# Kernel tuning notes

Hardware: AMD Instinct MI355X
Metric: run time of the kernel (lower is better)

## Reference

```python
import jax, jax.numpy as jnp
import numpy as np

N = 50000        # nodes
E = 800000       # edges
F_IN = 128       # input_nf == output_nf
HID = 128        # hidden_nf
HEADS = 4
HD = HID // HEADS            # 32 per-head hidden
FEAT = 2 * F_IN + 1 + 1 + 1 + 9   # 268 edge feature dim


def setup_inputs() -> dict:
    key = jax.random.key(0)
    ks = jax.random.split(key, 16)
    f32 = jnp.float32
    inp = {}
    inp["h"] = jax.random.normal(ks[0], (N, F_IN), dtype=f32)
    inp["coord"] = jax.random.normal(ks[1], (N, 3), dtype=f32)
    inp["edge_index"] = jax.random.randint(ks[2], (2, E), 0, N, dtype=jnp.int64 if jax.config.read('jax_enable_x64') else jnp.int32)
    # per-head edge MLP: Linear(FEAT,HD) -> SiLU -> Linear(HD,HD), stacked over heads
    inp["eW1"] = jax.random.normal(ks[3], (HEADS, FEAT, HD), dtype=f32) / np.sqrt(FEAT)
    inp["eb1"] = jnp.zeros((HEADS, HD), dtype=f32)
    inp["eW2"] = jax.random.normal(ks[4], (HEADS, HD, HD), dtype=f32) / np.sqrt(HD)
    inp["eb2"] = jnp.zeros((HEADS, HD), dtype=f32)
    # LayerNorm over hidden_nf
    inp["ln_g"] = jnp.ones((HID,), dtype=f32)
    inp["ln_b"] = jnp.zeros((HID,), dtype=f32)
    # node_mlp: Linear(HID+F_IN, HID) -> SiLU -> Linear(HID, F_IN)
    inp["nW1"] = jax.random.normal(ks[5], (HID + F_IN, HID), dtype=f32) / np.sqrt(HID + F_IN)
    inp["nb1"] = jnp.zeros((HID,), dtype=f32)
    inp["nW2"] = jax.random.normal(ks[6], (HID, F_IN), dtype=f32) / np.sqrt(HID)
    inp["nb2"] = jnp.zeros((F_IN,), dtype=f32)
    # coord_mlp: Linear(HID, HID) -> SiLU -> Linear(HID, 1, bias=False, xavier gain=0.001)
    inp["cW1"] = jax.random.normal(ks[7], (HID, HID), dtype=f32) / np.sqrt(HID)
    inp["cb1"] = jnp.zeros((HID,), dtype=f32)
    inp["cW2"] = jax.random.normal(ks[8], (HID, 1), dtype=f32) * 0.001
    return inp


def _forward(h, coord, edge_index, eW1, eb1, eW2, eb2, ln_g, ln_b,
             nW1, nb1, nW2, nb2, cW1, cb1, cW2):
    eps, thr = 1e-8, 1e-6
    row, col = edge_index[0], edge_index[1]
    n = h.shape[0]
    ci = coord[row]            # [E,3]
    ck = coord[col]            # [E,3]
    coord_diff = ci - ck       # rel_coord, also used for coord update
    radial = jnp.sum(coord_diff * coord_diff, axis=-1, keepdims=True)   # [E,1]
    dist = jnp.sqrt(radial)                                             # ||rel_coord||
    dot = jnp.sum(ci * ck, axis=-1, keepdims=True)                      # [E,1]
    # SO3 frame per edge
    a = coord_diff / (jnp.linalg.norm(coord_diff, axis=1, keepdims=True) + eps)
    cp = jnp.cross(ci, ck)
    b = cp / (jnp.linalg.norm(cp, axis=1, keepdims=True) + eps)
    c = jnp.cross(a, b)
    mask = ((jnp.linalg.norm(a, axis=1) < thr) |
            (jnp.linalg.norm(b, axis=1) < thr) |
            (jnp.linalg.norm(c, axis=1) < thr))
    so3 = jnp.stack([a, b, c], axis=2)                                  # [E,3,3] columns a,b,c
    so3 = jnp.where(mask[:, None, None], jnp.eye(3, dtype=so3.dtype), so3)
    so3_flat = so3.reshape(-1, 9)
    # edge features -> per-head small MLPs
    feats = jnp.concatenate([h[row], h[col], radial, dist, dot, so3_flat], axis=1)  # [E,FEAT]
    x = jax.nn.silu(jnp.einsum('ef,hfd->hed', feats, eW1) + eb1[:, None, :])
    x = jnp.einsum('hed,hdk->hek', x, eW2) + eb2[:, None, :]            # [H,E,HD]
    edge_feat = jnp.transpose(x, (1, 0, 2)).reshape(x.shape[1], -1)     # [E,HID], head-major concat
    # LayerNorm
    mu = edge_feat.mean(axis=-1, keepdims=True)
    var = edge_feat.var(axis=-1, keepdims=True)
    edge_feat = (edge_feat - mu) / jnp.sqrt(var + 1e-5) * ln_g + ln_b
    # coord update
    w = jax.nn.silu(edge_feat @ cW1 + cb1) @ cW2                        # [E,1]
    trans = coord_diff * w
    coord_out = coord + jax.ops.segment_sum(trans, row, num_segments=n)
    # node update
    agg = jax.ops.segment_sum(edge_feat, row, num_segments=n)           # [N,HID]
    y = jax.nn.silu(jnp.concatenate([h, agg], axis=1) @ nW1 + nb1) @ nW2 + nb2
    h_out = h + y                                                       # residual
    return h_out, coord_out


def reference(h, coord, edge_index, eW1, eb1, eW2, eb2, ln_g, ln_b,
              nW1, nb1, nW2, nb2, cW1, cb1, cW2):
    return _forward(h, coord, edge_index, eW1, eb1, eW2, eb2, ln_g, ln_b,
                    nW1, nb1, nW2, nb2, cW1, cb1, cW2)
```

## Files before the change

### kernel.cpp

```cpp
#include <hip/hip_runtime.h>
#include <hip/hip_bf16.h>
#include <math.h>

#define NN 50000
#define EE 800000
#define FIN 128
#define HIDN 128
#define HD 32
#define FEATD 268
#define K1 288
#define KP1 296
#define TE 64
#define TN2 64

typedef __bf16 bf16x8 __attribute__((ext_vector_type(8)));
typedef __bf16 bf16x4 __attribute__((ext_vector_type(4)));
typedef float  f32x4  __attribute__((ext_vector_type(4)));

#define MFMA(a, b, c) __builtin_amdgcn_mfma_f32_16x16x32_bf16((a), (b), (c), 0, 0, 0)

__device__ __forceinline__ float silu_f(float x) {
    return x / (1.0f + __expf(-x));
}

__global__ void wconv_kernel(const float* __restrict__ eW1, const float* __restrict__ eW2,
                             const float* __restrict__ cW1, const float* __restrict__ nW1,
                             const float* __restrict__ nW2,
                             __bf16* __restrict__ eW1t, __bf16* __restrict__ eW2t,
                             __bf16* __restrict__ cW1t, __bf16* __restrict__ nW1t,
                             __bf16* __restrict__ nW2t)
{
    const int i = blockIdx.x * 256 + threadIdx.x;
    if (i < 4 * 32 * K1) {
        const int hh = i / (32 * K1), rs = i % (32 * K1), d = rs / K1, k = rs % K1;
        const float v = (k < FEATD) ? eW1[(size_t)hh * FEATD * HD + (size_t)k * HD + d] : 0.f;
        eW1t[i] = (__bf16)v;
    }
    if (i < 4 * HD * HD) {
        const int hh = i / (HD * HD), rs = i % (HD * HD), d = rs / HD, k = rs % HD;
        eW2t[i] = (__bf16)eW2[(size_t)hh * HD * HD + (size_t)k * HD + d];
    }
    if (i < HIDN * HIDN) {
        const int o = i / HIDN, k = i % HIDN;
        cW1t[i] = (__bf16)cW1[(size_t)k * HIDN + o];
    }
    if (i < HIDN * (2 * FIN)) {
        const int o = i / (2 * FIN), k = i % (2 * FIN);
        nW1t[i] = (__bf16)nW1[(size_t)k * HIDN + o];
    }
    if (i < FIN * HIDN) {
        const int o = i / HIDN, k = i % HIDN;
        nW2t[i] = (__bf16)nW2[(size_t)k * FIN + o];
    }
}

__global__ __launch_bounds__(256) void hconv_kernel(const float* __restrict__ h,
                                                    float* __restrict__ houtbase)
{
    const int i = blockIdx.x * 256 + threadIdx.x;
    if (i >= NN * FIN / 8) return;
    const int row = i >> 4;
    const int c8  = i & 15;
    const float4* src = (const float4*)(h + (size_t)row * FIN + c8 * 8);
    float4 a = src[0], b = src[1];
    bf16x8 v = { (__bf16)a.x, (__bf16)a.y, (__bf16)a.z, (__bf16)a.w,
                 (__bf16)b.x, (__bf16)b.y, (__bf16)b.z, (__bf16)b.w };
    *(bf16x8*)((char*)houtbase + (size_t)row * 512 + c8 * 16) = v;
}

__global__ __launch_bounds__(512) void edge_kernel(
    const float* __restrict__ coord,
    const int* __restrict__ ei,
    const __bf16* __restrict__ eW1t, const float* __restrict__ eb1,
    const __bf16* __restrict__ eW2t, const float* __restrict__ eb2,
    const float* __restrict__ ln_g, const float* __restrict__ ln_b,
    const __bf16* __restrict__ cW1t, const float* __restrict__ cb1,
    const float* __restrict__ cW2,
    float* __restrict__ houtbase, float* __restrict__ coord_out)
{
    __shared__ __align__(16) unsigned char smemA[TE * KP1 * 2];
    __shared__ __align__(16) unsigned char smemB[4 * TE * 40 * 2];
    __shared__ float cdiff[TE][3];
    __shared__ int   rowlds[TE];
    __shared__ float wsum[TE];

    __bf16 (*featsB)[KP1] = (__bf16 (*)[KP1])smemA;
    float  (*efs)[132]    = (float  (*)[132])smemA;
    __bf16 (*efsB)[136]   = (__bf16 (*)[136])smemB;

    const int t  = threadIdx.x;
    const int e0 = blockIdx.x * TE;

    if (t < TE) wsum[t] = 0.f;

    {
        const int e = t >> 3;
        const int q = t & 7;
        const int r = ei[e0 + e];
        const int c = ei[EE + e0 + e];
        #pragma unroll
        for (int j = 0; j < 2; j++) {
            const int c16 = q + 8 * j;
            uint4 vr = *(const uint4*)((const char*)houtbase + (size_t)r * 512 + c16 * 16);
            *(uint4*)&featsB[e][c16 * 8] = vr;
            uint4 vc = *(const uint4*)((const char*)houtbase + (size_t)c * 512 + c16 * 16);
            *(uint4*)&featsB[e][FIN + c16 * 8] = vc;
        }
        if (q == 0) {
            rowlds[e] = r;
            const float cix = coord[(size_t)r*3+0], ciy = coord[(size_t)r*3+1], ciz = coord[(size_t)r*3+2];
            const float ckx = coord[(size_t)c*3+0], cky = coord[(size_t)c*3+1], ckz = coord[(size_t)c*3+2];
            const float dx = cix-ckx, dy = ciy-cky, dz = ciz-ckz;
            cdiff[e][0]=dx; cdiff[e][1]=dy; cdiff[e][2]=dz;
            const float radial = dx*dx + dy*dy + dz*dz;
            const float dist   = sqrtf(radial);
            const float dotv   = cix*ckx + ciy*cky + ciz*ckz;
            const float ia = 1.0f / (dist + 1e-8f);
            float ax = dx*ia, ay = dy*ia, az = dz*ia;
            const float cpx = ciy*ckz - ciz*cky;
            const float cpy = ciz*ckx - cix*ckz;
            const float cpz = cix*cky - ciy*ckx;
            const float cpn = sqrtf(cpx*cpx + cpy*cpy + cpz*cpz);
            const float ib = 1.0f / (cpn + 1e-8f);
            float bx = cpx*ib, by = cpy*ib, bz = cpz*ib;
            float cx = ay*bz - az*by;
            float cy = az*bx - ax*bz;
            float cz = ax*by - ay*bx;
            const float na = sqrtf(ax*ax + ay*ay + az*az);
            const float nb = sqrtf(bx*bx + by*by + bz*bz);
            const float nc = sqrtf(cx*cx + cy*cy + cz*cz);
            if (na < 1e-6f || nb < 1e-6f || nc < 1e-6f) {
                ax=1.f; bx=0.f; cx=0.f;
                ay=0.f; by=1.f; cy=0.f;
                az=0.f; bz=0.f; cz=1.f;
            }
            featsB[e][256]=(__bf16)radial; featsB[e][257]=(__bf16)dist; featsB[e][258]=(__bf16)dotv;
            featsB[e][259]=(__bf16)ax; featsB[e][260]=(__bf16)bx; featsB[e][261]=(__bf16)cx;
            featsB[e][262]=(__bf16)ay; featsB[e][263]=(__bf16)by; featsB[e][264]=(__bf16)cy;
            featsB[e][265]=(__bf16)az; featsB[e][266]=(__bf16)bz; featsB[e][267]=(__bf16)cz;
            #pragma unroll
            for (int k = FEATD; k < K1; k++) featsB[e][k] = (__bf16)0.f;
        }
    }
    __syncthreads();

    const int wv2  = t >> 6;
    const int hh   = wv2 >> 1;
    const int mh   = wv2 & 1;
    const int lane = t & 63;
    const int lr   = lane & 15;
    const int lg   = lane >> 4;

    __bf16* hidB = ((__bf16*)smemB) + hh * (TE * 40);

    const f32x4 z4 = { 0.f, 0.f, 0.f, 0.f };

    {
        f32x4 acc[2][2];
        #pragma unroll
        for (int mti = 0; mti < 2; mti++) { acc[mti][0] = z4; acc[mti][1] = z4; }
        const __bf16* W1 = eW1t + (size_t)hh * 32 * K1;
        #pragma unroll
        for (int ks = 0; ks < 9; ks++) {
            const int kof = ks * 32 + lg * 8;
            bf16x8 b0 = *(const bf16x8*)(W1 + (size_t)lr * K1 + kof);
            bf16x8 b1 = *(const bf16x8*)(W1 + (size_t)(16 + lr) * K1 + kof);
            #pragma unroll
            for (int mti = 0; mti < 2; mti++) {
                bf16x8 a = *(const bf16x8*)(&featsB[(mh * 2 + mti) * 16 + lr][kof]);
                acc[mti][0] = MFMA(a, b0, acc[mti][0]);
                acc[mti][1] = MFMA(a, b1, acc[mti][1]);
            }
        }
        const float b1a = eb1[hh * HD + lr];
        const float b1b = eb1[hh * HD + 16 + lr];
        #pragma unroll
        for (int mti = 0; mti < 2; mti++) {
            #pragma unroll
            for (int r = 0; r < 4; r++) {
                const int erow = (mh * 2 + mti) * 16 + lg * 4 + r;
                hidB[erow * 40 + lr]      = (__bf16)silu_f(acc[mti][0][r] + b1a);
                hidB[erow * 40 + 16 + lr] = (__bf16)silu_f(acc[mti][1][r] + b1b);
            }
        }
    }
    __syncthreads();

    {
        f32x4 acc2[2][2];
        #pragma unroll
        for (int mti = 0; mti < 2; mti++) { acc2[mti][0] = z4; acc2[mti][1] = z4; }
        const __bf16* W2 = eW2t + (size_t)hh * HD * HD;
        const int kof2 = lg * 8;
        bf16x8 b20 = *(const bf16x8*)(W2 + (size_t)lr * HD + kof2);
        bf16x8 b21 = *(const bf16x8*)(W2 + (size_t)(16 + lr) * HD + kof2);
        #pragma unroll
        for (int mti = 0; mti < 2; mti++) {
            bf16x8 a = *(const bf16x8*)(hidB + ((mh * 2 + mti) * 16 + lr) * 40 + kof2);
            acc2[mti][0] = MFMA(a, b20, acc2[mti][0]);
            acc2[mti][1] = MFMA(a, b21, acc2[mti][1]);
        }
        const float b2a = eb2[hh * HD + lr];
        const float b2b = eb2[hh * HD + 16 + lr];
        #pragma unroll
        for (int mti = 0; mti < 2; mti++) {
            #pragma unroll
            for (int r = 0; r < 4; r++) {
                const int erow = (mh * 2 + mti) * 16 + lg * 4 + r;
                efs[erow][hh * HD + lr]      = acc2[mti][0][r] + b2a;
                efs[erow][hh * HD + 16 + lr] = acc2[mti][1][r] + b2b;
            }
        }
    }
    __syncthreads();

    {
        const int el = t >> 3;
        const int q8 = t & 7;
        float s = 0.f, s2 = 0.f;
        #pragma unroll
        for (int i = 0; i < 16; i++) {
            const float v = efs[el][q8 + 8 * i];
            s += v; s2 += v * v;
        }
        s  += __shfl_xor(s, 1);  s  += __shfl_xor(s, 2);  s  += __shfl_xor(s, 4);
        s2 += __shfl_xor(s2, 1); s2 += __shfl_xor(s2, 2); s2 += __shfl_xor(s2, 4);
        const float mu   = s * (1.f / 128.f);
        const float var  = s2 * (1.f / 128.f) - mu * mu;
        const float rstd = rsqrtf(var + 1e-5f);
        #pragma unroll
        for (int i = 0; i < 16; i++) {
            const int oo = q8 + 8 * i;
            const float v  = efs[el][oo];
            const float nv = (v - mu) * rstd * ln_g[oo] + ln_b[oo];
            efsB[el][oo] = (__bf16)nv;
        }
    }
    __syncthreads();

    {
        f32x4 acc3[2][2];
        #pragma unroll
        for (int mti = 0; mti < 2; mti++) { acc3[mti][0] = z4; acc3[mti][1] = z4; }
        const __bf16* W3 = cW1t + (size_t)hh * 32 * HIDN;
        #pragma unroll
        for (int ks = 0; ks < 4; ks++) {
            const int kof = ks * 32 + lg * 8;
            bf16x8 b30 = *(const bf16x8*)(W3 + (size_t)lr * HIDN + kof);
            bf16x8 b31 = *(const bf16x8*)(W3 + (size_t)(16 + lr) * HIDN + kof);
            #pragma unroll
            for (int mti = 0; mti < 2; mti++) {
                bf16x8 a = *(const bf16x8*)(&efsB[(mh * 2 + mti) * 16 + lr][kof]);
                acc3[mti][0] = MFMA(a, b30, acc3[mti][0]);
                acc3[mti][1] = MFMA(a, b31, acc3[mti][1]);
            }
        }
        const int c0 = hh * 32 + lr, c1 = c0 + 16;
        const float cbA = cb1[c0], cbB = cb1[c1];
        const float cwA = cW2[c0], cwB = cW2[c1];
        float pe[8];
        #pragma unroll
        for (int mti = 0; mti < 2; mti++)
            #pragma unroll
            for (int r = 0; r < 4; r++)
                pe[mti * 4 + r] = silu_f(acc3[mti][0][r] + cbA) * cwA
                                + silu_f(acc3[mti][1][r] + cbB) * cwB;
        #pragma unroll
        for (int d = 1; d < 16; d <<= 1)
            #pragma unroll
            for (int i = 0; i < 8; i++) pe[i] += __shfl_xor(pe[i], d);
        if (lr == 0) {
            #pragma unroll
            for (int mti = 0; mti < 2; mti++)
                #pragma unroll
                for (int r = 0; r < 4; r++)
                    atomicAdd(&wsum[(mh * 2 + mti) * 16 + lg * 4 + r], pe[mti * 4 + r]);
        }
    }
    __syncthreads();

    if (t < TE) {
        const float we = wsum[t];
        const int r = rowlds[t];
        atomicAdd(&coord_out[(size_t)r*3+0], cdiff[t][0] * we);
        atomicAdd(&coord_out[(size_t)r*3+1], cdiff[t][1] * we);
        atomicAdd(&coord_out[(size_t)r*3+2], cdiff[t][2] * we);
    }

    {
        const int p  = t & 63;
        const int gq = t >> 6;
        #pragma unroll
        for (int e2 = 0; e2 < 8; e2++) {
            const int ee = gq * 8 + e2;
            __hip_bfloat162 pk = *(__hip_bfloat162*)&efsB[ee][2 * p];
            __hip_bfloat162* addr = (__hip_bfloat162*)
                ((char*)houtbase + (size_t)rowlds[ee] * 512 + 256 + p * 4);
            unsafeAtomicAdd(addr, pk);
        }
    }
}

__global__ __launch_bounds__(512) void node_kernel(
    const float* __restrict__ h,
    const __bf16* __restrict__ nW1t, const float* __restrict__ nb1,
    const __bf16* __restrict__ nW2t, const float* __restrict__ nb2,
    float* __restrict__ h_out)
{
    __shared__ __align__(16) __bf16 featsN[TN2][264];
    __shared__ __align__(16) __bf16 hidN[TN2][136];

    const int t  = threadIdx.x;
    const int n0 = blockIdx.x * TN2;

    {
        const int n = t >> 3;
        const int q = t & 7;
        const int nid = n0 + n;
        const bool ok = nid < NN;
        const uint4* rowp = (const uint4*)((const char*)h_out + (size_t)nid * 512);
        #pragma unroll
        for (int j = 0; j < 4; j++) {
            const int w4 = q * 4 + j;
            uint4 u = ok ? rowp[w4] : make_uint4(0u, 0u, 0u, 0u);
            *(uint4*)&featsN[n][w4 * 8] = u;
        }
    }
    __syncthreads();

    const int wv2  = t >> 6;
    const int hh2  = wv2 >> 1;
    const int mh   = wv2 & 1;
    const int lane = t & 63;
    const int lr   = lane & 15;
    const int lg   = lane >> 4;

    const f32x4 z4 = { 0.f, 0.f, 0.f, 0.f };

    {
        f32x4 acc[2][2];
        #pragma unroll
        for (int mti = 0; mti < 2; mti++) { acc[mti][0] = z4; acc[mti][1] = z4; }
        const __bf16* W1 = nW1t + (size_t)hh2 * 32 * 256;
        #pragma unroll
        for (int ks = 0; ks < 8; ks++) {
            const int kof = ks * 32 + lg * 8;
            bf16x8 b0 = *(const bf16x8*)(W1 + (size_t)lr * 256 + kof);
            bf16x8 b1 = *(const bf16x8*)(W1 + (size_t)(16 + lr) * 256 + kof);
            #pragma unroll
            for (int mti = 0; mti < 2; mti++) {
                bf16x8 a = *(const bf16x8*)(&featsN[(mh * 2 + mti) * 16 + lr][kof]);
                acc[mti][0] = MFMA(a, b0, acc[mti][0]);
                acc[mti][1] = MFMA(a, b1, acc[mti][1]);
            }
        }
        const float b1a = nb1[hh2 * 32 + lr];
        const float b1b = nb1[hh2 * 32 + 16 + lr];
        #pragma unroll
        for (int mti = 0; mti < 2; mti++) {
            #pragma unroll
            for (int r = 0; r < 4; r++) {
                const int erow = (mh * 2 + mti) * 16 + lg * 4 + r;
                hidN[erow][hh2 * 32 + lr]      = (__bf16)silu_f(acc[mti][0][r] + b1a);
                hidN[erow][hh2 * 32 + 16 + lr] = (__bf16)silu_f(acc[mti][1][r] + b1b);
            }
        }
    }
    __syncthreads();

    {
        f32x4 acc2[2][2];
        #pragma unroll
        for (int mti = 0; mti < 2; mti++) { acc2[mti][0] = z4; acc2[mti][1] = z4; }
        const __bf16* W2 = nW2t + (size_t)hh2 * 32 * 128;
        #pragma unroll
        for (int ks = 0; ks < 4; ks++) {
            const int kof = ks * 32 + lg * 8;
            bf16x8 b0 = *(const bf16x8*)(W2 + (size_t)lr * 128 + kof);
            bf16x8 b1 = *(const bf16x8*)(W2 + (size_t)(16 + lr) * 128 + kof);
            #pragma unroll
            for (int mti = 0; mti < 2; mti++) {
                bf16x8 a = *(const bf16x8*)(&hidN[(mh * 2 + mti) * 16 + lr][kof]);
                acc2[mti][0] = MFMA(a, b0, acc2[mti][0]);
                acc2[mti][1] = MFMA(a, b1, acc2[mti][1]);
            }
        }
        const float b2a = nb2[hh2 * 32 + lr];
        const float b2b = nb2[hh2 * 32 + 16 + lr];
        const int c0 = hh2 * 32 + lr, c1 = c0 + 16;
        #pragma unroll
        for (int mti = 0; mti < 2; mti++) {
            #pragma unroll
            for (int r = 0; r < 4; r++) {
                const int erow = (mh * 2 + mti) * 16 + lg * 4 + r;
                const int nid  = n0 + erow;
                if (nid < NN) {
                    h_out[(size_t)nid * FIN + c0] = h[(size_t)nid * FIN + c0] + acc2[mti][0][r] + b2a;
                    h_out[(size_t)nid * FIN + c1] = h[(size_t)nid * FIN + c1] + acc2[mti][1][r] + b2b;
                }
            }
        }
    }
}

extern "C" void kernel_launch(void* const* d_in, const int* in_sizes, int n_in,
                              void* d_out, int out_size, void* d_ws, size_t ws_size,
                              hipStream_t stream)
{
    (void)in_sizes; (void)n_in; (void)out_size; (void)ws_size;
    const float* h     = (const float*)d_in[0];
    const float* coord = (const float*)d_in[1];
    const int*   ei    = (const int*)d_in[2];
    const float* eW1   = (const float*)d_in[3];
    const float* eb1   = (const float*)d_in[4];
    const float* eW2   = (const float*)d_in[5];
    const float* eb2   = (const float*)d_in[6];
    const float* ln_g  = (const float*)d_in[7];
    const float* ln_b  = (const float*)d_in[8];
    const float* nW1   = (const float*)d_in[9];
    const float* nb1   = (const float*)d_in[10];
    const float* nW2   = (const float*)d_in[11];
    const float* nb2   = (const float*)d_in[12];
    const float* cW1   = (const float*)d_in[13];
    const float* cb1   = (const float*)d_in[14];
    const float* cW2   = (const float*)d_in[15];

    float* h_out     = (float*)d_out;
    float* coord_out = h_out + (size_t)NN * FIN;

    __bf16* eW1t = (__bf16*)d_ws;
    __bf16* eW2t = eW1t + 4 * 32 * K1;
    __bf16* cW1t = eW2t + 4 * HD * HD;
    __bf16* nW1t = cW1t + HIDN * HIDN;
    __bf16* nW2t = nW1t + HIDN * (2 * FIN);

    hipMemsetAsync(h_out, 0, (size_t)NN * FIN * sizeof(float), stream);
    hipMemcpyAsync(coord_out, coord, (size_t)NN * 3 * sizeof(float),
                   hipMemcpyDeviceToDevice, stream);
    wconv_kernel<<<(4 * 32 * K1 + 255) / 256, 256, 0, stream>>>(
        eW1, eW2, cW1, nW1, nW2, eW1t, eW2t, cW1t, nW1t, nW2t);
    hconv_kernel<<<(NN * FIN / 8 + 255) / 256, 256, 0, stream>>>(h, h_out);

    edge_kernel<<<EE / TE, 512, 0, stream>>>(coord, ei, eW1t, eb1, eW2t, eb2,
                                             ln_g, ln_b, cW1t, cb1, cW2,
                                             h_out, coord_out);
    node_kernel<<<(NN + TN2 - 1) / TN2, 512, 0, stream>>>(h, nW1t, nb1, nW2t, nb2, h_out);
}
```

Before: 435.6 us.

## Load gathered node features directly into MFMA operands and fuse LayerNorm stats into registers

The edge kernel no longer stages the gathered bf16 h rows into a large shared-memory feature tile. Each lane now reads its MFMA A-operand fragments straight from global memory for the row and column nodes, and only the small geometric features stay in LDS. LayerNorm statistics are reduced with shuffles and LDS atomics while the values stay in registers, which removes the fp32 efs staging buffer and one barrier pass. This cuts LDS usage and should raise occupancy. The cost is that each of the four head-waves re-reads the same gathered rows from global/L2, so gather traffic is duplicated four times.

```diff
diff --git a/kernel.cpp b/kernel.cpp
--- a/kernel.cpp
+++ b/kernel.cpp
@@ -9,12 +9,10 @@
 #define HD 32
 #define FEATD 268
 #define K1 288
-#define KP1 296
 #define TE 64
 #define TN2 64
 
 typedef __bf16 bf16x8 __attribute__((ext_vector_type(8)));
-typedef __bf16 bf16x4 __attribute__((ext_vector_type(4)));
 typedef float  f32x4  __attribute__((ext_vector_type(4)));
 
 #define MFMA(a, b, c) __builtin_amdgcn_mfma_f32_16x16x32_bf16((a), (b), (c), 0, 0, 0)
@@ -78,69 +76,57 @@
     const float* __restrict__ cW2,
     float* __restrict__ houtbase, float* __restrict__ coord_out)
 {
-    __shared__ __align__(16) unsigned char smemA[TE * KP1 * 2];
+    __shared__ __align__(16) __bf16 geomB[TE][40];
     __shared__ __align__(16) unsigned char smemB[4 * TE * 40 * 2];
+    __shared__ int   rowlds[TE];
+    __shared__ int   collds[TE];
     __shared__ float cdiff[TE][3];
-    __shared__ int   rowlds[TE];
     __shared__ float wsum[TE];
-
-    __bf16 (*featsB)[KP1] = (__bf16 (*)[KP1])smemA;
-    float  (*efs)[132]    = (float  (*)[132])smemA;
-    __bf16 (*efsB)[136]   = (__bf16 (*)[136])smemB;
+    __shared__ float lnS[TE][2];
+
+    __bf16 (*efsB)[136] = (__bf16 (*)[136])smemB;
 
     const int t  = threadIdx.x;
     const int e0 = blockIdx.x * TE;
 
-    if (t < TE) wsum[t] = 0.f;
-
-    {
-        const int e = t >> 3;
-        const int q = t & 7;
+    if (t < TE) {
+        const int e = t;
         const int r = ei[e0 + e];
         const int c = ei[EE + e0 + e];
-        #pragma unroll
-        for (int j = 0; j < 2; j++) {
-            const int c16 = q + 8 * j;
-            uint4 vr = *(const uint4*)((const char*)houtbase + (size_t)r * 512 + c16 * 16);
-            *(uint4*)&featsB[e][c16 * 8] = vr;
-            uint4 vc = *(const uint4*)((const char*)houtbase + (size_t)c * 512 + c16 * 16);
-            *(uint4*)&featsB[e][FIN + c16 * 8] = vc;
-        }
-        if (q == 0) {
-            rowlds[e] = r;
-            const float cix = coord[(size_t)r*3+0], ciy = coord[(size_t)r*3+1], ciz = coord[(size_t)r*3+2];
-            const float ckx = coord[(size_t)c*3+0], cky = coord[(size_t)c*3+1], ckz = coord[(size_t)c*3+2];
-            const float dx = cix-ckx, dy = ciy-cky, dz = ciz-ckz;
-            cdiff[e][0]=dx; cdiff[e][1]=dy; cdiff[e][2]=dz;
-            const float radial = dx*dx + dy*dy + dz*dz;
-            const float dist   = sqrtf(radial);
-            const float dotv   = cix*ckx + ciy*cky + ciz*ckz;
-            const float ia = 1.0f / (dist + 1e-8f);
-            float ax = dx*ia, ay = dy*ia, az = dz*ia;
-            const float cpx = ciy*ckz - ciz*cky;
-            const float cpy = ciz*ckx - cix*ckz;
-            const float cpz = cix*cky - ciy*ckx;
-            const float cpn = sqrtf(cpx*cpx + cpy*cpy + cpz*cpz);
-            const float ib = 1.0f / (cpn + 1e-8f);
-            float bx = cpx*ib, by = cpy*ib, bz = cpz*ib;
-            float cx = ay*bz - az*by;
-            float cy = az*bx - ax*bz;
-            float cz = ax*by - ay*bx;
-            const float na = sqrtf(ax*ax + ay*ay + az*az);
-            const float nb = sqrtf(bx*bx + by*by + bz*bz);
-            const float nc = sqrtf(cx*cx + cy*cy + cz*cz);
-            if (na < 1e-6f || nb < 1e-6f || nc < 1e-6f) {
-                ax=1.f; bx=0.f; cx=0.f;
-                ay=0.f; by=1.f; cy=0.f;
-                az=0.f; bz=0.f; cz=1.f;
-            }
-            featsB[e][256]=(__bf16)radial; featsB[e][257]=(__bf16)dist; featsB[e][258]=(__bf16)dotv;
-            featsB[e][259]=(__bf16)ax; featsB[e][260]=(__bf16)bx; featsB[e][261]=(__bf16)cx;
-            featsB[e][262]=(__bf16)ay; featsB[e][263]=(__bf16)by; featsB[e][264]=(__bf16)cy;
-            featsB[e][265]=(__bf16)az; featsB[e][266]=(__bf16)bz; featsB[e][267]=(__bf16)cz;
-            #pragma unroll
-            for (int k = FEATD; k < K1; k++) featsB[e][k] = (__bf16)0.f;
-        }
+        rowlds[e] = r; collds[e] = c;
+        wsum[e] = 0.f; lnS[e][0] = 0.f; lnS[e][1] = 0.f;
+        const float cix = coord[(size_t)r*3+0], ciy = coord[(size_t)r*3+1], ciz = coord[(size_t)r*3+2];
+        const float ckx = coord[(size_t)c*3+0], cky = coord[(size_t)c*3+1], ckz = coord[(size_t)c*3+2];
+        const float dx = cix-ckx, dy = ciy-cky, dz = ciz-ckz;
+        cdiff[e][0]=dx; cdiff[e][1]=dy; cdiff[e][2]=dz;
+        const float radial = dx*dx + dy*dy + dz*dz;
+        const float dist   = sqrtf(radial);
+        const float dotv   = cix*ckx + ciy*cky + ciz*ckz;
+        const float ia = 1.0f / (dist + 1e-8f);
+        float ax = dx*ia, ay = dy*ia, az = dz*ia;
+        const float cpx = ciy*ckz - ciz*cky;
+        const float cpy = ciz*ckx - cix*ckz;
+        const float cpz = cix*cky - ciy*ckx;
+        const float cpn = sqrtf(cpx*cpx + cpy*cpy + cpz*cpz);
+        const float ib = 1.0f / (cpn + 1e-8f);
+        float bx = cpx*ib, by = cpy*ib, bz = cpz*ib;
+        float cx = ay*bz - az*by;
+        float cy = az*bx - ax*bz;
+        float cz = ax*by - ay*bx;
+        const float na = sqrtf(ax*ax + ay*ay + az*az);
+        const float nb = sqrtf(bx*bx + by*by + bz*bz);
+        const float nc = sqrtf(cx*cx + cy*cy + cz*cz);
+        if (na < 1e-6f || nb < 1e-6f || nc < 1e-6f) {
+            ax=1.f; bx=0.f; cx=0.f;
+            ay=0.f; by=1.f; cy=0.f;
+            az=0.f; bz=0.f; cz=1.f;
+        }
+        geomB[e][0]=(__bf16)radial; geomB[e][1]=(__bf16)dist; geomB[e][2]=(__bf16)dotv;
+        geomB[e][3]=(__bf16)ax; geomB[e][4]=(__bf16)bx; geomB[e][5]=(__bf16)cx;
+        geomB[e][6]=(__bf16)ay; geomB[e][7]=(__bf16)by; geomB[e][8]=(__bf16)cy;
+        geomB[e][9]=(__bf16)az; geomB[e][10]=(__bf16)bz; geomB[e][11]=(__bf16)cz;
+        #pragma unroll
+        for (int k = 12; k < 32; k++) geomB[e][k] = (__bf16)0.f;
     }
     __syncthreads();
 
@@ -150,12 +136,21 @@
     const int lane = t & 63;
     const int lr   = lane & 15;
     const int lg   = lane >> 4;
+    const int mhbase = mh * 32;
 
     __bf16* hidB = ((__bf16*)smemB) + hh * (TE * 40);
 
     const f32x4 z4 = { 0.f, 0.f, 0.f, 0.f };
 
     {
+        const char* base_r[2];
+        const char* base_c[2];
+        #pragma unroll
+        for (int mti = 0; mti < 2; mti++) {
+            const int erow = mhbase + mti * 16 + lr;
+            base_r[mti] = (const char*)houtbase + (size_t)rowlds[erow] * 512 + lg * 16;
+            base_c[mti] = (const char*)houtbase + (size_t)collds[erow] * 512 + lg * 16;
+        }
         f32x4 acc[2][2];
         #pragma unroll
         for (int mti = 0; mti < 2; mti++) { acc[mti][0] = z4; acc[mti][1] = z4; }
@@ -167,7 +162,10 @@
             bf16x8 b1 = *(const bf16x8*)(W1 + (size_t)(16 + lr) * K1 + kof);
             #pragma unroll
             for (int mti = 0; mti < 2; mti++) {
-                bf16x8 a = *(const bf16x8*)(&featsB[(mh * 2 + mti) * 16 + lr][kof]);
+                bf16x8 a;
+                if (ks < 4)      a = *(const bf16x8*)(base_r[mti] + ks * 64);
+                else if (ks < 8) a = *(const bf16x8*)(base_c[mti] + (ks - 4) * 64);
+                else             a = *(const bf16x8*)(&geomB[mhbase + mti * 16 + lr][lg * 8]);
                 acc[mti][0] = MFMA(a, b0, acc[mti][0]);
                 acc[mti][1] = MFMA(a, b1, acc[mti][1]);
             }
@@ -178,7 +176,7 @@
         for (int mti = 0; mti < 2; mti++) {
             #pragma unroll
             for (int r = 0; r < 4; r++) {
-                const int erow = (mh * 2 + mti) * 16 + lg * 4 + r;
+                const int erow = (mhbase + mti * 16) + lg * 4 + r;
                 hidB[erow * 40 + lr]      = (__bf16)silu_f(acc[mti][0][r] + b1a);
                 hidB[erow * 40 + 16 + lr] = (__bf16)silu_f(acc[mti][1][r] + b1b);
             }
@@ -186,6 +184,7 @@
     }
     __syncthreads();
 
+    float val[2][2][4];
     {
         f32x4 acc2[2][2];
         #pragma unroll
@@ -196,7 +195,7 @@
         bf16x8 b21 = *(const bf16x8*)(W2 + (size_t)(16 + lr) * HD + kof2);
         #pragma unroll
         for (int mti = 0; mti < 2; mti++) {
-            bf16x8 a = *(const bf16x8*)(hidB + ((mh * 2 + mti) * 16 + lr) * 40 + kof2);
+            bf16x8 a = *(const bf16x8*)(hidB + ((mhbase + mti * 16) + lr) * 40 + kof2);
             acc2[mti][0] = MFMA(a, b20, acc2[mti][0]);
             acc2[mti][1] = MFMA(a, b21, acc2[mti][1]);
         }
@@ -206,34 +205,40 @@
         for (int mti = 0; mti < 2; mti++) {
             #pragma unroll
             for (int r = 0; r < 4; r++) {
-                const int erow = (mh * 2 + mti) * 16 + lg * 4 + r;
-                efs[erow][hh * HD + lr]      = acc2[mti][0][r] + b2a;
-                efs[erow][hh * HD + 16 + lr] = acc2[mti][1][r] + b2b;
-            }
-        }
-    }
-    __syncthreads();
-
-    {
-        const int el = t >> 3;
-        const int q8 = t & 7;
-        float s = 0.f, s2 = 0.f;
-        #pragma unroll
-        for (int i = 0; i < 16; i++) {
-            const float v = efs[el][q8 + 8 * i];
-            s += v; s2 += v * v;
-        }
-        s  += __shfl_xor(s, 1);  s  += __shfl_xor(s, 2);  s  += __shfl_xor(s, 4);
-        s2 += __shfl_xor(s2, 1); s2 += __shfl_xor(s2, 2); s2 += __shfl_xor(s2, 4);
-        const float mu   = s * (1.f / 128.f);
-        const float var  = s2 * (1.f / 128.f) - mu * mu;
-        const float rstd = rsqrtf(var + 1e-5f);
-        #pragma unroll
-        for (int i = 0; i < 16; i++) {
-            const int oo = q8 + 8 * i;
-            const float v  = efs[el][oo];
-            const float nv = (v - mu) * rstd * ln_g[oo] + ln_b[oo];
-            efsB[el][oo] = (__bf16)nv;
+                val[mti][0][r] = acc2[mti][0][r] + b2a;
+                val[mti][1][r] = acc2[mti][1][r] + b2b;
+                float s  = val[mti][0][r] + val[mti][1][r];
+                float s2 = val[mti][0][r] * val[mti][0][r]
+                         + val[mti][1][r] * val[mti][1][r];
+                s  += __shfl_xor(s, 1);  s2 += __shfl_xor(s2, 1);
+                s  += __shfl_xor(s, 2);  s2 += __shfl_xor(s2, 2);
+                s  += __shfl_xor(s, 4);  s2 += __shfl_xor(s2, 4);
+                s  += __shfl_xor(s, 8);  s2 += __shfl_xor(s2, 8);
+                if (lr == 0) {
+                    const int erow = (mhbase + mti * 16) + lg * 4 + r;
+                    atomicAdd(&lnS[erow][0], s);
+                    atomicAdd(&lnS[erow][1], s2);
+                }
+            }
+        }
+    }
+    __syncthreads();
+
+    {
+        const int c0 = hh * 32 + lr, c1 = c0 + 16;
+        const float g0 = ln_g[c0], bl0 = ln_b[c0];
+        const float g1 = ln_g[c1], bl1 = ln_b[c1];
+        #pragma unroll
+        for (int mti = 0; mti < 2; mti++) {
+            #pragma unroll
+            for (int r = 0; r < 4; r++) {
+                const int erow = (mhbase + mti * 16) + lg * 4 + r;
+                const float mu   = lnS[erow][0] * (1.f / 128.f);
+                const float var  = lnS[erow][1] * (1.f / 128.f) - mu * mu;
+                const float rstd = rsqrtf(var + 1e-5f);
+                efsB[erow][c0] = (__bf16)((val[mti][0][r] - mu) * rstd * g0 + bl0);
+                efsB[erow][c1] = (__bf16)((val[mti][1][r] - mu) * rstd * g1 + bl1);
+            }
         }
     }
     __syncthreads();
@@ -250,7 +255,7 @@
             bf16x8 b31 = *(const bf16x8*)(W3 + (size_t)(16 + lr) * HIDN + kof);
             #pragma unroll
             for (int mti = 0; mti < 2; mti++) {
-                bf16x8 a = *(const bf16x8*)(&efsB[(mh * 2 + mti) * 16 + lr][kof]);
+                bf16x8 a = *(const bf16x8*)(&efsB[(mhbase + mti * 16) + lr][kof]);
                 acc3[mti][0] = MFMA(a, b30, acc3[mti][0]);
                 acc3[mti][1] = MFMA(a, b31, acc3[mti][1]);
             }
@@ -274,7 +279,7 @@
             for (int mti = 0; mti < 2; mti++)
                 #pragma unroll
                 for (int r = 0; r < 4; r++)
-                    atomicAdd(&wsum[(mh * 2 + mti) * 16 + lg * 4 + r], pe[mti * 4 + r]);
+                    atomicAdd(&wsum[(mhbase + mti * 16) + lg * 4 + r], pe[mti * 4 + r]);
         }
     }
     __syncthreads();
```

Measured after the change: 496.3 us. 13.9% more time.

## Restructure edge kernel to one wave per 16 edges with register-resident features

Applied to the files above, without the earlier changes.

The edge kernel now gives each wavefront its own 16 edges and has it run all four heads, the LayerNorm and the coord MLP. Block-wide __syncthreads and the large shared staging buffers go away. Gathered node features are loaded straight into MFMA A-operand registers, and LayerNorm is done in registers with lane shuffles. The aim is to cut barrier stalls and LDS traffic and to raise occupancy through smaller blocks and less shared memory. In exchange, each wave reloads all weight B-fragments for every head, which adds more global/L2 weight reads per edge.

```diff
diff --git a/kernel.cpp b/kernel.cpp
--- a/kernel.cpp
+++ b/kernel.cpp
@@ -9,12 +9,9 @@
 #define HD 32
 #define FEATD 268
 #define K1 288
-#define KP1 296
-#define TE 64
 #define TN2 64
 
 typedef __bf16 bf16x8 __attribute__((ext_vector_type(8)));
-typedef __bf16 bf16x4 __attribute__((ext_vector_type(4)));
 typedef float  f32x4  __attribute__((ext_vector_type(4)));
 
 #define MFMA(a, b, c) __builtin_amdgcn_mfma_f32_16x16x32_bf16((a), (b), (c), 0, 0, 0)
@@ -68,7 +65,7 @@
     *(bf16x8*)((char*)houtbase + (size_t)row * 512 + c8 * 16) = v;
 }
 
-__global__ __launch_bounds__(512) void edge_kernel(
+__global__ __launch_bounds__(256) void edge_kernel(
     const float* __restrict__ coord,
     const int* __restrict__ ei,
     const __bf16* __restrict__ eW1t, const float* __restrict__ eb1,
@@ -78,225 +75,200 @@
     const float* __restrict__ cW2,
     float* __restrict__ houtbase, float* __restrict__ coord_out)
 {
-    __shared__ __align__(16) unsigned char smemA[TE * KP1 * 2];
-    __shared__ __align__(16) unsigned char smemB[4 * TE * 40 * 2];
-    __shared__ float cdiff[TE][3];
-    __shared__ int   rowlds[TE];
-    __shared__ float wsum[TE];
-
-    __bf16 (*featsB)[KP1] = (__bf16 (*)[KP1])smemA;
-    float  (*efs)[132]    = (float  (*)[132])smemA;
-    __bf16 (*efsB)[136]   = (__bf16 (*)[136])smemB;
-
-    const int t  = threadIdx.x;
-    const int e0 = blockIdx.x * TE;
-
-    if (t < TE) wsum[t] = 0.f;
-
-    {
-        const int e = t >> 3;
-        const int q = t & 7;
-        const int r = ei[e0 + e];
-        const int c = ei[EE + e0 + e];
-        #pragma unroll
-        for (int j = 0; j < 2; j++) {
-            const int c16 = q + 8 * j;
-            uint4 vr = *(const uint4*)((const char*)houtbase + (size_t)r * 512 + c16 * 16);
-            *(uint4*)&featsB[e][c16 * 8] = vr;
-            uint4 vc = *(const uint4*)((const char*)houtbase + (size_t)c * 512 + c16 * 16);
-            *(uint4*)&featsB[e][FIN + c16 * 8] = vc;
-        }
-        if (q == 0) {
-            rowlds[e] = r;
-            const float cix = coord[(size_t)r*3+0], ciy = coord[(size_t)r*3+1], ciz = coord[(size_t)r*3+2];
-            const float ckx = coord[(size_t)c*3+0], cky = coord[(size_t)c*3+1], ckz = coord[(size_t)c*3+2];
-            const float dx = cix-ckx, dy = ciy-cky, dz = ciz-ckz;
-            cdiff[e][0]=dx; cdiff[e][1]=dy; cdiff[e][2]=dz;
-            const float radial = dx*dx + dy*dy + dz*dz;
-            const float dist   = sqrtf(radial);
-            const float dotv   = cix*ckx + ciy*cky + ciz*ckz;
-            const float ia = 1.0f / (dist + 1e-8f);
-            float ax = dx*ia, ay = dy*ia, az = dz*ia;
-            const float cpx = ciy*ckz - ciz*cky;
-            const float cpy = ciz*ckx - cix*ckz;
-            const float cpz = cix*cky - ciy*ckx;
-            const float cpn = sqrtf(cpx*cpx + cpy*cpy + cpz*cpz);
-            const float ib = 1.0f / (cpn + 1e-8f);
-            float bx = cpx*ib, by = cpy*ib, bz = cpz*ib;
-            float cx = ay*bz - az*by;
-            float cy = az*bx - ax*bz;
-            float cz = ax*by - ay*bx;
-            const float na = sqrtf(ax*ax + ay*ay + az*az);
-            const float nb = sqrtf(bx*bx + by*by + bz*bz);
-            const float nc = sqrtf(cx*cx + cy*cy + cz*cz);
-            if (na < 1e-6f || nb < 1e-6f || nc < 1e-6f) {
-                ax=1.f; bx=0.f; cx=0.f;
-                ay=0.f; by=1.f; cy=0.f;
-                az=0.f; bz=0.f; cz=1.f;
-            }
-            featsB[e][256]=(__bf16)radial; featsB[e][257]=(__bf16)dist; featsB[e][258]=(__bf16)dotv;
-            featsB[e][259]=(__bf16)ax; featsB[e][260]=(__bf16)bx; featsB[e][261]=(__bf16)cx;
-            featsB[e][262]=(__bf16)ay; featsB[e][263]=(__bf16)by; featsB[e][264]=(__bf16)cy;
-            featsB[e][265]=(__bf16)az; featsB[e][266]=(__bf16)bz; featsB[e][267]=(__bf16)cz;
-            #pragma unroll
-            for (int k = FEATD; k < K1; k++) featsB[e][k] = (__bf16)0.f;
-        }
-    }
-    __syncthreads();
-
-    const int wv2  = t >> 6;
-    const int hh   = wv2 >> 1;
-    const int mh   = wv2 & 1;
+    __shared__ __align__(16) __bf16 geomS[4][16][40];
+    __shared__ __align__(16) __bf16 hidS[4][16][136];
+
+    const int t    = threadIdx.x;
+    const int w    = t >> 6;
     const int lane = t & 63;
     const int lr   = lane & 15;
     const int lg   = lane >> 4;
-
-    __bf16* hidB = ((__bf16*)smemB) + hh * (TE * 40);
+    const int ebase = blockIdx.x * 64 + w * 16;
+
+    __bf16 (*geomW)[40]  = geomS[w];
+    __bf16 (*hidW)[136]  = hidS[w];
+
+    int rI = 0, cI = 0;
+    float cdx = 0.f, cdy = 0.f, cdz = 0.f;
+    if (lane < 16) {
+        rI = ei[ebase + lane];
+        cI = ei[EE + ebase + lane];
+        const float cix = coord[(size_t)rI*3+0], ciy = coord[(size_t)rI*3+1], ciz = coord[(size_t)rI*3+2];
+        const float ckx = coord[(size_t)cI*3+0], cky = coord[(size_t)cI*3+1], ckz = coord[(size_t)cI*3+2];
+        cdx = cix-ckx; cdy = ciy-cky; cdz = ciz-ckz;
+        const float radial = cdx*cdx + cdy*cdy + cdz*cdz;
+        const float dist   = sqrtf(radial);
+        const float dotv   = cix*ckx + ciy*cky + ciz*ckz;
+        const float ia = 1.0f / (dist + 1e-8f);
+        float ax = cdx*ia, ay = cdy*ia, az = cdz*ia;
+        const float cpx = ciy*ckz - ciz*cky;
+        const float cpy = ciz*ckx - cix*ckz;
+        const float cpz = cix*cky - ciy*ckx;
+        const float cpn = sqrtf(cpx*cpx + cpy*cpy + cpz*cpz);
+        const float ib = 1.0f / (cpn + 1e-8f);
+        float bx = cpx*ib, by = cpy*ib, bz = cpz*ib;
+        float cx = ay*bz - az*by;
+        float cy = az*bx - ax*bz;
+        float cz = ax*by - ay*bx;
+        const float na = sqrtf(ax*ax + ay*ay + az*az);
+        const float nb = sqrtf(bx*bx + by*by + bz*bz);
+        const float nc = sqrtf(cx*cx + cy*cy + cz*cz);
+        if (na < 1e-6f || nb < 1e-6f || nc < 1e-6f) {
+            ax=1.f; bx=0.f; cx=0.f;
+            ay=0.f; by=1.f; cy=0.f;
+            az=0.f; bz=0.f; cz=1.f;
+        }
+        geomW[lane][0]=(__bf16)radial; geomW[lane][1]=(__bf16)dist; geomW[lane][2]=(__bf16)dotv;
+        geomW[lane][3]=(__bf16)ax; geomW[lane][4]=(__bf16)bx; geomW[lane][5]=(__bf16)cx;
+        geomW[lane][6]=(__bf16)ay; geomW[lane][7]=(__bf16)by; geomW[lane][8]=(__bf16)cy;
+        geomW[lane][9]=(__bf16)az; geomW[lane][10]=(__bf16)bz; geomW[lane][11]=(__bf16)cz;
+        #pragma unroll
+        for (int k = 12; k < 32; k++) geomW[lane][k] = (__bf16)0.f;
+    }
+    const int rB = __shfl(rI, lr);
+    const int cB = __shfl(cI, lr);
+
+    bf16x8 aF[9];
+    {
+        const char* pr = (const char*)houtbase + (size_t)rB * 512 + lg * 16;
+        const char* pc = (const char*)houtbase + (size_t)cB * 512 + lg * 16;
+        #pragma unroll
+        for (int ks = 0; ks < 4; ks++) aF[ks]     = *(const bf16x8*)(pr + ks * 64);
+        #pragma unroll
+        for (int ks = 0; ks < 4; ks++) aF[4 + ks] = *(const bf16x8*)(pc + ks * 64);
+        aF[8] = *(const bf16x8*)(&geomW[lr][lg * 8]);
+    }
 
     const f32x4 z4 = { 0.f, 0.f, 0.f, 0.f };
 
-    {
-        f32x4 acc[2][2];
-        #pragma unroll
-        for (int mti = 0; mti < 2; mti++) { acc[mti][0] = z4; acc[mti][1] = z4; }
+    #pragma unroll
+    for (int hh = 0; hh < 4; hh++) {
+        f32x4 acc0 = z4, acc1 = z4;
         const __bf16* W1 = eW1t + (size_t)hh * 32 * K1;
         #pragma unroll
         for (int ks = 0; ks < 9; ks++) {
             const int kof = ks * 32 + lg * 8;
             bf16x8 b0 = *(const bf16x8*)(W1 + (size_t)lr * K1 + kof);
             bf16x8 b1 = *(const bf16x8*)(W1 + (size_t)(16 + lr) * K1 + kof);
-            #pragma unroll
-            for (int mti = 0; mti < 2; mti++) {
-                bf16x8 a = *(const bf16x8*)(&featsB[(mh * 2 + mti) * 16 + lr][kof]);
-                acc[mti][0] = MFMA(a, b0, acc[mti][0]);
-                acc[mti][1] = MFMA(a, b1, acc[mti][1]);
-            }
+            acc0 = MFMA(aF[ks], b0, acc0);
+            acc1 = MFMA(aF[ks], b1, acc1);
         }
         const float b1a = eb1[hh * HD + lr];
         const float b1b = eb1[hh * HD + 16 + lr];
         #pragma unroll
-        for (int mti = 0; mti < 2; mti++) {
-            #pragma unroll
-            for (int r = 0; r < 4; r++) {
-                const int erow = (mh * 2 + mti) * 16 + lg * 4 + r;
-                hidB[erow * 40 + lr]      = (__bf16)silu_f(acc[mti][0][r] + b1a);
-                hidB[erow * 40 + 16 + lr] = (__bf16)silu_f(acc[mti][1][r] + b1b);
-            }
-        }
-    }
-    __syncthreads();
-
-    {
-        f32x4 acc2[2][2];
-        #pragma unroll
-        for (int mti = 0; mti < 2; mti++) { acc2[mti][0] = z4; acc2[mti][1] = z4; }
+        for (int r = 0; r < 4; r++) {
+            const int erow = lg * 4 + r;
+            hidW[erow][hh * 32 + lr]      = (__bf16)silu_f(acc0[r] + b1a);
+            hidW[erow][hh * 32 + 16 + lr] = (__bf16)silu_f(acc1[r] + b1b);
+        }
+    }
+
+    float val[4][2][4];
+    #pragma unroll
+    for (int hh = 0; hh < 4; hh++) {
+        f32x4 acc0 = z4, acc1 = z4;
         const __bf16* W2 = eW2t + (size_t)hh * HD * HD;
         const int kof2 = lg * 8;
         bf16x8 b20 = *(const bf16x8*)(W2 + (size_t)lr * HD + kof2);
         bf16x8 b21 = *(const bf16x8*)(W2 + (size_t)(16 + lr) * HD + kof2);
-        #pragma unroll
-        for (int mti = 0; mti < 2; mti++) {
-            bf16x8 a = *(const bf16x8*)(hidB + ((mh * 2 + mti) * 16 + lr) * 40 + kof2);
-            acc2[mti][0] = MFMA(a, b20, acc2[mti][0]);
-            acc2[mti][1] = MFMA(a, b21, acc2[mti][1]);
-        }
+        bf16x8 a = *(const bf16x8*)(&hidW[lr][hh * 32 + kof2]);
+        acc0 = MFMA(a, b20, acc0);
+        acc1 = MFMA(a, b21, acc1);
         const float b2a = eb2[hh * HD + lr];
         const float b2b = eb2[hh * HD + 16 + lr];
         #pragma unroll
-        for (int mti = 0; mti < 2; mti++) {
+        for (int r = 0; r < 4; r++) {
+            val[hh][0][r] = acc0[r] + b2a;
+            val[hh][1][r] = acc1[r] + b2b;
+        }
+    }
+
+    {
+        float gg[4][2], bb[4][2];
+        #pragma unroll
+        for (int hh = 0; hh < 4; hh++) {
+            gg[hh][0] = ln_g[hh * 32 + lr];      bb[hh][0] = ln_b[hh * 32 + lr];
+            gg[hh][1] = ln_g[hh * 32 + 16 + lr]; bb[hh][1] = ln_b[hh * 32 + 16 + lr];
+        }
+        #pragma unroll
+        for (int r = 0; r < 4; r++) {
+            float s = 0.f, s2 = 0.f;
+            #pragma unroll
+            for (int hh = 0; hh < 4; hh++) {
+                s  += val[hh][0][r] + val[hh][1][r];
+                s2 += val[hh][0][r] * val[hh][0][r] + val[hh][1][r] * val[hh][1][r];
+            }
+            s  += __shfl_xor(s, 1);  s2 += __shfl_xor(s2, 1);
+            s  += __shfl_xor(s, 2);  s2 += __shfl_xor(s2, 2);
+            s  += __shfl_xor(s, 4);  s2 += __shfl_xor(s2, 4);
+            s  += __shfl_xor(s, 8);  s2 += __shfl_xor(s2, 8);
+            const float mu   = s * (1.f / 128.f);
+            const float var  = s2 * (1.f / 128.f) - mu * mu;
+            const float rstd = rsqrtf(var + 1e-5f);
+            const int erow = lg * 4 + r;
+            #pragma unroll
+            for (int hh = 0; hh < 4; hh++) {
+                hidW[erow][hh * 32 + lr]      = (__bf16)((val[hh][0][r] - mu) * rstd * gg[hh][0] + bb[hh][0]);
+                hidW[erow][hh * 32 + 16 + lr] = (__bf16)((val[hh][1][r] - mu) * rstd * gg[hh][1] + bb[hh][1]);
+            }
+        }
+    }
+
+    {
+        const int eA = lane >> 2;
+        const int rA = __shfl(rI, eA);
+        char* dst = (char*)houtbase + (size_t)rA * 512 + 256;
+        #pragma unroll
+        for (int j = 0; j < 16; j++) {
+            const int p = (lane & 3) + 4 * j;
+            __hip_bfloat162 pk = *(__hip_bfloat162*)((char*)&hidW[eA][0] + p * 4);
+            unsafeAtomicAdd((__hip_bfloat162*)(dst + p * 4), pk);
+        }
+    }
+
+    {
+        bf16x8 a3[4];
+        #pragma unroll
+        for (int ks = 0; ks < 4; ks++)
+            a3[ks] = *(const bf16x8*)(&hidW[lr][ks * 32 + lg * 8]);
+        float pe[4] = {0.f, 0.f, 0.f, 0.f};
+        #pragma unroll
+        for (int cg = 0; cg < 8; cg++) {
+            f32x4 acc3 = z4;
+            const __bf16* W3 = cW1t + (size_t)(cg * 16 + lr) * HIDN;
+            #pragma unroll
+            for (int ks = 0; ks < 4; ks++) {
+                bf16x8 b = *(const bf16x8*)(W3 + ks * 32 + lg * 8);
+                acc3 = MFMA(a3[ks], b, acc3);
+            }
+            const int c = cg * 16 + lr;
+            const float cb = cb1[c];
+            const float cw = cW2[c];
+            #pragma unroll
+            for (int r = 0; r < 4; r++)
+                pe[r] += silu_f(acc3[r] + cb) * cw;
+        }
+        #pragma unroll
+        for (int d = 1; d < 16; d <<= 1) {
+            #pragma unroll
+            for (int r = 0; r < 4; r++) pe[r] += __shfl_xor(pe[r], d);
+        }
+        float cde[4][3]; int rEe[4];
+        #pragma unroll
+        for (int r = 0; r < 4; r++) {
+            const int e = lg * 4 + r;
+            rEe[r]    = __shfl(rI, e);
+            cde[r][0] = __shfl(cdx, e);
+            cde[r][1] = __shfl(cdy, e);
+            cde[r][2] = __shfl(cdz, e);
+        }
+        if (lr == 0) {
             #pragma unroll
             for (int r = 0; r < 4; r++) {
-                const int erow = (mh * 2 + mti) * 16 + lg * 4 + r;
-                efs[erow][hh * HD + lr]      = acc2[mti][0][r] + b2a;
-                efs[erow][hh * HD + 16 + lr] = acc2[mti][1][r] + b2b;
-            }
-        }
-    }
-    __syncthreads();
-
-    {
-        const int el = t >> 3;
-        const int q8 = t & 7;
-        float s = 0.f, s2 = 0.f;
-        #pragma unroll
-        for (int i = 0; i < 16; i++) {
-            const float v = efs[el][q8 + 8 * i];
-            s += v; s2 += v * v;
-        }
-        s  += __shfl_xor(s, 1);  s  += __shfl_xor(s, 2);  s  += __shfl_xor(s, 4);
-        s2 += __shfl_xor(s2, 1); s2 += __shfl_xor(s2, 2); s2 += __shfl_xor(s2, 4);
-        const float mu   = s * (1.f / 128.f);
-        const float var  = s2 * (1.f / 128.f) - mu * mu;
-        const float rstd = rsqrtf(var + 1e-5f);
-        #pragma unroll
-        for (int i = 0; i < 16; i++) {
-            const int oo = q8 + 8 * i;
-            const float v  = efs[el][oo];
-            const float nv = (v - mu) * rstd * ln_g[oo] + ln_b[oo];
-            efsB[el][oo] = (__bf16)nv;
-        }
-    }
-    __syncthreads();
-
-    {
-        f32x4 acc3[2][2];
-        #pragma unroll
-        for (int mti = 0; mti < 2; mti++) { acc3[mti][0] = z4; acc3[mti][1] = z4; }
-        const __bf16* W3 = cW1t + (size_t)hh * 32 * HIDN;
-        #pragma unroll
-        for (int ks = 0; ks < 4; ks++) {
-            const int kof = ks * 32 + lg * 8;
-            bf16x8 b30 = *(const bf16x8*)(W3 + (size_t)lr * HIDN + kof);
-            bf16x8 b31 = *(const bf16x8*)(W3 + (size_t)(16 + lr) * HIDN + kof);
-            #pragma unroll
-            for (int mti = 0; mti < 2; mti++) {
-                bf16x8 a = *(const bf16x8*)(&efsB[(mh * 2 + mti) * 16 + lr][kof]);
-                acc3[mti][0] = MFMA(a, b30, acc3[mti][0]);
-                acc3[mti][1] = MFMA(a, b31, acc3[mti][1]);
-            }
-        }
-        const int c0 = hh * 32 + lr, c1 = c0 + 16;
-        const float cbA = cb1[c0], cbB = cb1[c1];
-        const float cwA = cW2[c0], cwB = cW2[c1];
-        float pe[8];
-        #pragma unroll
-        for (int mti = 0; mti < 2; mti++)
-            #pragma unroll
-            for (int r = 0; r < 4; r++)
-                pe[mti * 4 + r] = silu_f(acc3[mti][0][r] + cbA) * cwA
-                                + silu_f(acc3[mti][1][r] + cbB) * cwB;
-        #pragma unroll
-        for (int d = 1; d < 16; d <<= 1)
-            #pragma unroll
-            for (int i = 0; i < 8; i++) pe[i] += __shfl_xor(pe[i], d);
-        if (lr == 0) {
-            #pragma unroll
-            for (int mti = 0; mti < 2; mti++)
-                #pragma unroll
-                for (int r = 0; r < 4; r++)
-                    atomicAdd(&wsum[(mh * 2 + mti) * 16 + lg * 4 + r], pe[mti * 4 + r]);
-        }
-    }
-    __syncthreads();
-
-    if (t < TE) {
-        const float we = wsum[t];
-        const int r = rowlds[t];
-        atomicAdd(&coord_out[(size_t)r*3+0], cdiff[t][0] * we);
-        atomicAdd(&coord_out[(size_t)r*3+1], cdiff[t][1] * we);
-        atomicAdd(&coord_out[(size_t)r*3+2], cdiff[t][2] * we);
-    }
-
-    {
-        const int p  = t & 63;
-        const int gq = t >> 6;
-        #pragma unroll
-        for (int e2 = 0; e2 < 8; e2++) {
-            const int ee = gq * 8 + e2;
-            __hip_bfloat162 pk = *(__hip_bfloat162*)&efsB[ee][2 * p];
-            __hip_bfloat162* addr = (__hip_bfloat162*)
-                ((char*)houtbase + (size_t)rowlds[ee] * 512 + 256 + p * 4);
-            unsafeAtomicAdd(addr, pk);
+                atomicAdd(&coord_out[(size_t)rEe[r]*3+0], cde[r][0] * pe[r]);
+                atomicAdd(&coord_out[(size_t)rEe[r]*3+1], cde[r][1] * pe[r]);
+                atomicAdd(&coord_out[(size_t)rEe[r]*3+2], cde[r][2] * pe[r]);
+            }
         }
     }
 }
@@ -441,7 +413,7 @@
         eW1, eW2, cW1, nW1, nW2, eW1t, eW2t, cW1t, nW1t, nW2t);
     hconv_kernel<<<(NN * FIN / 8 + 255) / 256, 256, 0, stream>>>(h, h_out);
 
-    edge_kernel<<<EE / TE, 512, 0, stream>>>(coord, ei, eW1t, eb1, eW2t, eb2,
+    edge_kernel<<<EE / 64, 256, 0, stream>>>(coord, ei, eW1t, eb1, eW2t, eb2,
                                              ln_g, ln_b, cW1t, cb1, cW2,
                                              h_out, coord_out);
     node_kernel<<<(NN + TN2 - 1) / TN2, 512, 0, stream>>>(h, nW1t, nb1, nW2t, nb2, h_out);
```

Measured after the change: 932.8 us. 2.14x slower.
